# Performance work log

Hardware: AMD Instinct MI355X
Metric: run time of the kernel (lower is better)

Reference implementation:

```python
import jax, jax.numpy as jnp
import numpy as np

D = 1024  # embed_dim

def setup_inputs() -> dict:
    key = jax.random.key(0)
    ks = jax.random.split(key, 5)
    s = 1.0 / np.sqrt(D)  # keep weight magnitudes sane
    x = jax.random.normal(ks[0], (2, 4096, D), dtype=jnp.float32)
    Wq = jax.random.normal(ks[1], (D, D), dtype=jnp.float32) * s
    Wk = jax.random.normal(ks[2], (D, D), dtype=jnp.float32) * s
    Wv = jax.random.normal(ks[3], (D, D), dtype=jnp.float32) * s
    Wo = jax.random.normal(ks[4], (D, D), dtype=jnp.float32) * s
    return {"x": x, "Wq": Wq, "Wk": Wk, "Wv": Wv, "Wo": Wo}

def reference(x, Wq, Wk, Wv, Wo):
    # torch nn.Linear(no bias): y = x @ W.T
    q = jnp.einsum('bsd,ed->bse', x, Wq)
    k = jnp.einsum('bsd,ed->bse', x, Wk)
    v = jnp.einsum('bsd,ed->bse', x, Wv)
    embed_dim = x.shape[-1]
    scores = jnp.einsum('bqd,bkd->bqk', q, k) / jnp.sqrt(jnp.asarray(embed_dim, x.dtype))
    attn = jax.nn.softmax(scores, axis=-1)  # dropout is identity in eval mode (p=0)
    out = jnp.einsum('bqk,bkd->bqd', attn, v)
    out = jnp.einsum('bsd,ed->bse', out, Wo)
    return out
```

## Files before the change

### kernel.cpp

```cpp
#include <hip/hip_runtime.h>
#include <hip/hip_bf16.h>

using short8 = __attribute__((ext_vector_type(8))) short;
using f32x4  = __attribute__((ext_vector_type(4))) float;

__device__ __forceinline__ unsigned short f2bf(float f) {
  union { float f; unsigned int u; } x; x.f = f;
  unsigned int r = (x.u + 0x7fffu + ((x.u >> 16) & 1u)) >> 16;
  return (unsigned short)r;
}

__device__ __forceinline__ void gld_lds16(const short* gp, short* lp) {
  __builtin_amdgcn_global_load_lds((const __attribute__((address_space(1))) void*)gp,
                                   (__attribute__((address_space(3))) void*)lp, 16, 0, 0);
}

__global__ __launch_bounds__(256) void cast_all(const float* __restrict__ x,
                                                const float* __restrict__ Wq,
                                                const float* __restrict__ Wk,
                                                const float* __restrict__ Wv,
                                                const float* __restrict__ Wo,
                                                short* __restrict__ xb,
                                                short* __restrict__ wqkv,
                                                short* __restrict__ wo,
                                                short* __restrict__ wvT,
                                                float4* __restrict__ sums4) {
  const int bid = blockIdx.x;
  const int tid = threadIdx.x;
  if (bid < 11264) {
    const float4* src;
    short* dst;
    const int i = bid * 256 + tid;
    if (bid < 8192) {
      src = (const float4*)x + i;
      dst = xb + 4ll * i;
    } else {
      const int j = i - 2097152;
      const int w = j >> 18;
      const int off = j & 262143;
      src = (const float4*)(w == 0 ? Wq : w == 1 ? Wk : Wo) + off;
      dst = (w == 0 ? wqkv : w == 1 ? wqkv + 1048576 : wo) + 4ll * off;
    }
    float4 f = *src;
    short4 o;
    o.x = (short)f2bf(f.x); o.y = (short)f2bf(f.y);
    o.z = (short)f2bf(f.z); o.w = (short)f2bf(f.w);
    *(short4*)dst = o;
    if (bid < 8) sums4[bid * 256 + tid] = float4{0.f, 0.f, 0.f, 0.f};
  } else {
    __shared__ short tls[64][65];
    const int t  = bid - 11264;
    const int bx = t & 15, by = t >> 4;
    const int r  = tid >> 4;
    const int c4 = (tid & 15) * 4;
#pragma unroll
    for (int s = 0; s < 4; ++s) {
      float4 f = *(const float4*)(Wv + (long long)(by * 64 + r + s * 16) * 1024 + bx * 64 + c4);
      tls[r + s * 16][c4 + 0] = (short)f2bf(f.x);
      tls[r + s * 16][c4 + 1] = (short)f2bf(f.y);
      tls[r + s * 16][c4 + 2] = (short)f2bf(f.z);
      tls[r + s * 16][c4 + 3] = (short)f2bf(f.w);
    }
    __syncthreads();
#pragma unroll
    for (int s = 0; s < 4; ++s) {
      const int a = r + s * 16;
      short4 o;
      o.x = tls[c4 + 0][a]; o.y = tls[c4 + 1][a];
      o.z = tls[c4 + 2][a]; o.w = tls[c4 + 3][a];
      *(short4*)(wvT + (long long)(bx * 64 + a) * 1024 + by * 64 + c4) = o;
    }
  }
}

template <int MODE>
__global__ __launch_bounds__(256) void gemm_bt(const short* __restrict__ A,
                                               const short* __restrict__ B,
                                               void* __restrict__ Cv,
                                               float* __restrict__ sums,
                                               int K, int ldc, float scale,
                                               long long aStr, long long bStr,
                                               long long cStr, int gy, int ng) {
  __shared__ short lA[128 * 64];
  __shared__ short lB[128 * 64];
  const int bid = blockIdx.x;
  const int bx  = bid / ng;
  const int g   = bid % ng;
  const int by  = g % gy;
  const long long z = g / gy;
  const int tid = threadIdx.x;
  const int w   = tid >> 6;
  const int l   = tid & 63;
  const int wm  = w >> 1, wn = w & 1;
  const long long tm = (long long)by * 128;
  const long long tn = (long long)bx * 128;
  A += z * aStr;
  B += z * bStr;

  const bool swp = (MODE == 2) ? (bx < 16) : true;

  f32x4 acc[4][4] = {};

  const int lr   = l >> 3;
  const int scw  = ((l & 7) ^ (lr & 7)) * 8;
  const int q4   = l >> 4;
  const int fr   = l & 15;
  const int xr   = fr & 7;

  for (int k0 = 0; k0 < K; k0 += 64) {
#pragma unroll
    for (int t = 0; t < 4; ++t) {
      const int seg = w * 4 + t;
      gld_lds16(A + (tm + seg * 8 + lr) * (long long)K + k0 + scw, &lA[seg * 512]);
      gld_lds16(B + (tn + seg * 8 + lr) * (long long)K + k0 + scw, &lB[seg * 512]);
    }
    __syncthreads();
#pragma unroll
    for (int kk = 0; kk < 64; kk += 32) {
      const int cs = ((((kk >> 3)) + q4) ^ xr) << 3;
      short8 af[4], bfr[4];
#pragma unroll
      for (int i = 0; i < 4; ++i)
        af[i] = *(const short8*)&lA[(wm * 64 + i * 16 + fr) * 64 + cs];
#pragma unroll
      for (int j = 0; j < 4; ++j)
        bfr[j] = *(const short8*)&lB[(wn * 64 + j * 16 + fr) * 64 + cs];
      if (swp) {
#pragma unroll
        for (int i = 0; i < 4; ++i)
#pragma unroll
          for (int j = 0; j < 4; ++j)
            acc[i][j] = __builtin_amdgcn_mfma_f32_16x16x32_bf16(bfr[j], af[i], acc[i][j], 0, 0, 0);
      } else {
#pragma unroll
        for (int i = 0; i < 4; ++i)
#pragma unroll
          for (int j = 0; j < 4; ++j)
            acc[i][j] = __builtin_amdgcn_mfma_f32_16x16x32_bf16(af[i], bfr[j], acc[i][j], 0, 0, 0);
      }
    }
    __syncthreads();
  }

  const int rb = (l >> 4) * 4;

  if (MODE == 1) {
    unsigned short* dst = (unsigned short*)Cv + z * cStr;
#pragma unroll
    for (int i = 0; i < 4; ++i) {
      const long long row = tm + wm * 64 + i * 16 + fr;
#pragma unroll
      for (int j = 0; j < 4; ++j) {
        const long long colb = tn + wn * 64 + j * 16 + rb;
        short4 pk;
        pk.x = (short)f2bf(acc[i][j][0]); pk.y = (short)f2bf(acc[i][j][1]);
        pk.z = (short)f2bf(acc[i][j][2]); pk.w = (short)f2bf(acc[i][j][3]);
        *(short4*)(dst + row * ldc + colb) = pk;
      }
    }
  } else if (MODE == 2) {
    const int cb0 = (int)(tn & 1023) + wn * 64;
    if (swp) {
      const int region = (int)(tn >> 10);
      unsigned short* dst = (unsigned short*)Cv + (long long)region * 8388608ll;
#pragma unroll
      for (int i = 0; i < 4; ++i) {
        const long long row = tm + wm * 64 + i * 16 + fr;
#pragma unroll
        for (int j = 0; j < 4; ++j) {
          const int colb = cb0 + j * 16 + rb;
          short4 pk;
          pk.x = (short)f2bf(acc[i][j][0]); pk.y = (short)f2bf(acc[i][j][1]);
          pk.z = (short)f2bf(acc[i][j][2]); pk.w = (short)f2bf(acc[i][j][3]);
          *(short4*)(dst + row * 1024 + colb) = pk;
        }
      }
    } else {
      unsigned short* dst = (unsigned short*)Cv + 16777216ll;
#pragma unroll
      for (int i = 0; i < 4; ++i)
#pragma unroll
        for (int j = 0; j < 4; ++j) {
          const long long row0 = tm + wm * 64 + i * 16 + rb;
          const long long b = row0 >> 12, s0 = row0 & 4095;
          const int c = cb0 + j * 16 + fr;
          short4 pk;
          pk.x = (short)f2bf(acc[i][j][0]); pk.y = (short)f2bf(acc[i][j][1]);
          pk.z = (short)f2bf(acc[i][j][2]); pk.w = (short)f2bf(acc[i][j][3]);
          *(short4*)(dst + b * 4194304ll + (long long)c * 4096 + s0) = pk;
        }
    }
  } else if (MODE == 4) {
    unsigned short* dst = (unsigned short*)Cv + z * cStr;
    float* sm = sums + z * 4096;
#pragma unroll
    for (int i = 0; i < 4; ++i) {
      const long long row = tm + wm * 64 + i * 16 + fr;
      float rs = 0.f;
#pragma unroll
      for (int j = 0; j < 4; ++j) {
        const long long colb = tn + wn * 64 + j * 16 + rb;
        short4 pk;
        float e0 = __expf(acc[i][j][0] * scale);
        float e1 = __expf(acc[i][j][1] * scale);
        float e2 = __expf(acc[i][j][2] * scale);
        float e3 = __expf(acc[i][j][3] * scale);
        rs += (e0 + e1) + (e2 + e3);
        pk.x = (short)f2bf(e0); pk.y = (short)f2bf(e1);
        pk.z = (short)f2bf(e2); pk.w = (short)f2bf(e3);
        *(short4*)(dst + row * ldc + colb) = pk;
      }
      rs += __shfl_xor(rs, 16);
      rs += __shfl_xor(rs, 32);
      if (l < 16) atomicAdd(sm + tm + wm * 64 + i * 16 + l, rs);
    }
  } else {
    float* dst = (float*)Cv + z * cStr;
    const float* sm = sums + z * 4096;
#pragma unroll
    for (int i = 0; i < 4; ++i) {
      const long long row = tm + wm * 64 + i * 16 + fr;
      const float inv = 1.0f / sm[row];
#pragma unroll
      for (int j = 0; j < 4; ++j) {
        const long long colb = tn + wn * 64 + j * 16 + rb;
        f32x4 o;
        o[0] = acc[i][j][0] * inv; o[1] = acc[i][j][1] * inv;
        o[2] = acc[i][j][2] * inv; o[3] = acc[i][j][3] * inv;
        *(f32x4*)(dst + row * ldc + colb) = o;
      }
    }
  }
}

extern "C" void kernel_launch(void* const* d_in, const int* in_sizes, int n_in,
                              void* d_out, int out_size, void* d_ws, size_t ws_size,
                              hipStream_t stream) {
  const float* x  = (const float*)d_in[0];
  const float* Wq = (const float*)d_in[1];
  const float* Wk = (const float*)d_in[2];
  const float* Wv = (const float*)d_in[3];
  const float* Wo = (const float*)d_in[4];
  float* out = (float*)d_out;

  char* ws = (char*)d_ws;
  short* xb   = (short*)ws;
  short* wqkv = (short*)(ws + (16ll << 20));
  short* wo   = wqkv + 3145728;
  short* q    = (short*)(ws + (24ll << 20));
  short* k    = q + 8388608;
  short* vt   = q + 16777216;
  float* sums = (float*)(ws + (72ll << 20));
  short* wvT  = (short*)(ws + (88ll << 20));
  short* sc   = (short*)(ws + (88ll << 20));
  short* wvo  = wqkv + 2097152;

  const bool batched = ws_size >= 159383552ull;
  dim3 blk(256);

  cast_all<<<11520, blk, 0, stream>>>(x, Wq, Wk, Wv, Wo, xb, wqkv, wo, wvT,
                                      (float4*)sums);

  gemm_bt<1><<<8 * 8, blk, 0, stream>>>(wo, wvT, wvo, nullptr, 1024, 1024, 1.f,
                                        0, 0, 0, 8, 8);

  gemm_bt<2><<<24 * 64, blk, 0, stream>>>(xb, wqkv, q, nullptr, 1024, 1024, 1.f,
                                          0, 0, 0, 64, 64);

  if (batched) {
    gemm_bt<4><<<32 * 64, blk, 0, stream>>>(q, k, sc, sums, 1024, 4096, 0.03125f,
                                            4194304ll, 4194304ll, 16777216ll, 32, 64);
    gemm_bt<6><<<8 * 64, blk, 0, stream>>>(sc, vt, out, sums, 4096, 1024, 1.f,
                                           16777216ll, 4194304ll, 4194304ll, 32, 64);
  } else {
    for (int b = 0; b < 2; ++b) {
      short* qb  = q  + (long long)b * 4194304;
      short* kb  = k  + (long long)b * 4194304;
      short* vb  = vt + (long long)b * 4194304;
      float* ob  = out + (long long)b * 4194304;
      float* smb = sums + (long long)b * 4096;
      gemm_bt<4><<<32 * 32, blk, 0, stream>>>(qb, kb, sc, smb, 1024, 4096, 0.03125f,
                                              0, 0, 0, 32, 32);
      gemm_bt<6><<<8 * 32, blk, 0, stream>>>(sc, vb, ob, smb, 4096, 1024, 1.f,
                                             0, 0, 0, 32, 32);
    }
  }
}
```

Measured before the change: 348.8 us.

## Fold Wk into query projection to drop the separate K projection GEMM

Precomputes Wk^T·Wq alongside Wo·Wv as a batched weight-only GEMM, then projects x once through the fused Wq-Wk product and the Wo·Wv product. The score GEMM uses bf16 x directly in place of K, so the x·Wk^T projection (a third of the QKV GEMM) and its K buffer disappear. The cast kernel now transposes Wq, Wk and Wv into the layouts the weight GEMM needs. The extra rounding through the fused bf16 weights may shift numerics slightly.

```diff
diff --git a/kernel.cpp b/kernel.cpp
--- a/kernel.cpp
+++ b/kernel.cpp
@@ -21,13 +21,12 @@
                                                 const float* __restrict__ Wv,
                                                 const float* __restrict__ Wo,
                                                 short* __restrict__ xb,
-                                                short* __restrict__ wqkv,
-                                                short* __restrict__ wo,
-                                                short* __restrict__ wvT,
+                                                short* __restrict__ U,
+                                                short* __restrict__ V,
                                                 float4* __restrict__ sums4) {
   const int bid = blockIdx.x;
   const int tid = threadIdx.x;
-  if (bid < 11264) {
+  if (bid < 9216) {
     const float4* src;
     short* dst;
     const int i = bid * 256 + tid;
@@ -35,11 +34,9 @@
       src = (const float4*)x + i;
       dst = xb + 4ll * i;
     } else {
-      const int j = i - 2097152;
-      const int w = j >> 18;
-      const int off = j & 262143;
-      src = (const float4*)(w == 0 ? Wq : w == 1 ? Wk : Wo) + off;
-      dst = (w == 0 ? wqkv : w == 1 ? wqkv + 1048576 : wo) + 4ll * off;
+      const int off = i - 2097152;
+      src = (const float4*)Wo + off;
+      dst = U + 1048576 + 4ll * off;
     }
     float4 f = *src;
     short4 o;
@@ -49,13 +46,17 @@
     if (bid < 8) sums4[bid * 256 + tid] = float4{0.f, 0.f, 0.f, 0.f};
   } else {
     __shared__ short tls[64][65];
-    const int t  = bid - 11264;
-    const int bx = t & 15, by = t >> 4;
+    const int t  = bid - 9216;
+    const int w  = t >> 8;
+    const int ti = t & 255;
+    const int bx = ti & 15, by = ti >> 4;
+    const float* src = (w == 0) ? Wq : (w == 1) ? Wk : Wv;
+    short* dst = (w == 0) ? V : (w == 1) ? U : V + 1048576;
     const int r  = tid >> 4;
     const int c4 = (tid & 15) * 4;
 #pragma unroll
     for (int s = 0; s < 4; ++s) {
-      float4 f = *(const float4*)(Wv + (long long)(by * 64 + r + s * 16) * 1024 + bx * 64 + c4);
+      float4 f = *(const float4*)(src + (long long)(by * 64 + r + s * 16) * 1024 + bx * 64 + c4);
       tls[r + s * 16][c4 + 0] = (short)f2bf(f.x);
       tls[r + s * 16][c4 + 1] = (short)f2bf(f.y);
       tls[r + s * 16][c4 + 2] = (short)f2bf(f.z);
@@ -68,7 +69,7 @@
       short4 o;
       o.x = tls[c4 + 0][a]; o.y = tls[c4 + 1][a];
       o.z = tls[c4 + 2][a]; o.w = tls[c4 + 3][a];
-      *(short4*)(wvT + (long long)(bx * 64 + a) * 1024 + by * 64 + c4) = o;
+      *(short4*)(dst + (long long)(bx * 64 + a) * 1024 + by * 64 + c4) = o;
     }
   }
 }
@@ -97,7 +98,7 @@
   A += z * aStr;
   B += z * bStr;
 
-  const bool swp = (MODE == 2) ? (bx < 16) : true;
+  const bool swp = (MODE == 2) ? (bx < 8) : true;
 
   f32x4 acc[4][4] = {};
 
@@ -159,10 +160,9 @@
       }
     }
   } else if (MODE == 2) {
-    const int cb0 = (int)(tn & 1023) + wn * 64;
     if (swp) {
-      const int region = (int)(tn >> 10);
-      unsigned short* dst = (unsigned short*)Cv + (long long)region * 8388608ll;
+      unsigned short* dst = (unsigned short*)Cv;
+      const int cb0 = (int)tn + wn * 64;
 #pragma unroll
       for (int i = 0; i < 4; ++i) {
         const long long row = tm + wm * 64 + i * 16 + fr;
@@ -176,7 +176,8 @@
         }
       }
     } else {
-      unsigned short* dst = (unsigned short*)Cv + 16777216ll;
+      unsigned short* dst = (unsigned short*)Cv + 8388608ll;
+      const int cb0 = (int)(tn - 1024) + wn * 64;
 #pragma unroll
       for (int i = 0; i < 4; ++i)
 #pragma unroll
@@ -244,42 +245,39 @@
   float* out = (float*)d_out;
 
   char* ws = (char*)d_ws;
-  short* xb   = (short*)ws;
-  short* wqkv = (short*)(ws + (16ll << 20));
-  short* wo   = wqkv + 3145728;
-  short* q    = (short*)(ws + (24ll << 20));
-  short* k    = q + 8388608;
-  short* vt   = q + 16777216;
-  float* sums = (float*)(ws + (72ll << 20));
-  short* wvT  = (short*)(ws + (88ll << 20));
-  short* sc   = (short*)(ws + (88ll << 20));
-  short* wvo  = wqkv + 2097152;
+  short* xb = (short*)ws;
+  short* U  = (short*)(ws + (16ll << 20));
+  short* V  = (short*)(ws + (20ll << 20));
+  short* W2 = (short*)(ws + (24ll << 20));
+  short* t  = (short*)(ws + (28ll << 20));
+  short* vt = t + 8388608;
+  float* sums = (float*)(ws + (60ll << 20));
+  short* sc = (short*)(ws + (88ll << 20));
 
   const bool batched = ws_size >= 159383552ull;
   dim3 blk(256);
 
-  cast_all<<<11520, blk, 0, stream>>>(x, Wq, Wk, Wv, Wo, xb, wqkv, wo, wvT,
-                                      (float4*)sums);
-
-  gemm_bt<1><<<8 * 8, blk, 0, stream>>>(wo, wvT, wvo, nullptr, 1024, 1024, 1.f,
-                                        0, 0, 0, 8, 8);
-
-  gemm_bt<2><<<24 * 64, blk, 0, stream>>>(xb, wqkv, q, nullptr, 1024, 1024, 1.f,
+  cast_all<<<9984, blk, 0, stream>>>(x, Wq, Wk, Wv, Wo, xb, U, V, (float4*)sums);
+
+  gemm_bt<1><<<8 * 16, blk, 0, stream>>>(U, V, W2, nullptr, 1024, 1024, 1.f,
+                                         1048576ll, 1048576ll, 1048576ll, 8, 16);
+
+  gemm_bt<2><<<16 * 64, blk, 0, stream>>>(xb, W2, t, nullptr, 1024, 1024, 1.f,
                                           0, 0, 0, 64, 64);
 
   if (batched) {
-    gemm_bt<4><<<32 * 64, blk, 0, stream>>>(q, k, sc, sums, 1024, 4096, 0.03125f,
+    gemm_bt<4><<<32 * 64, blk, 0, stream>>>(t, xb, sc, sums, 1024, 4096, 0.03125f,
                                             4194304ll, 4194304ll, 16777216ll, 32, 64);
     gemm_bt<6><<<8 * 64, blk, 0, stream>>>(sc, vt, out, sums, 4096, 1024, 1.f,
                                            16777216ll, 4194304ll, 4194304ll, 32, 64);
   } else {
     for (int b = 0; b < 2; ++b) {
-      short* qb  = q  + (long long)b * 4194304;
-      short* kb  = k  + (long long)b * 4194304;
+      short* tb  = t  + (long long)b * 4194304;
+      short* xbb = xb + (long long)b * 4194304;
       short* vb  = vt + (long long)b * 4194304;
       float* ob  = out + (long long)b * 4194304;
       float* smb = sums + (long long)b * 4096;
-      gemm_bt<4><<<32 * 32, blk, 0, stream>>>(qb, kb, sc, smb, 1024, 4096, 0.03125f,
+      gemm_bt<4><<<32 * 32, blk, 0, stream>>>(tb, xbb, sc, smb, 1024, 4096, 0.03125f,
                                               0, 0, 0, 32, 32);
       gemm_bt<6><<<8 * 32, blk, 0, stream>>>(sc, vb, ob, smb, 4096, 1024, 1.f,
                                              0, 0, 0, 32, 32);
```

Measured after the change: 318.5 us. -8.7%, faster.
